# Performance work log

Measured on AMD Instinct MI355X. Metric: run time of the kernel, lower is better.

The kernel has to match this reference:

```python
import jax, jax.numpy as jnp
import numpy as np

D = 64          # embedding_dim
B = 1024        # batch (queries)
R = 128         # num_relations
N = 100000      # num_nodes
E = 6400000     # num_edges


def setup_inputs() -> dict:
    key = jax.random.key(0)
    ks = jax.random.split(key, 16)
    inp = {
        "relation_embeddings": jax.random.normal(ks[0], (B, R, D), dtype=jnp.float32),
        "query_rels": jax.random.randint(ks[1], (B,), 0, R),
        "query_entities": jax.random.randint(ks[2], (B,), 0, N),
        "edge_index": jax.random.randint(ks[3], (2, E), 0, N),
        "edge_type": jax.random.randint(ks[4], (E,), 0, R),
        "num_nodes": N,
        # feature_extractor: Linear(2D+4 -> D), ReLU, Linear(D -> D//2), ReLU
        "W1": jax.random.normal(ks[5], (2 * D + 4, D), dtype=jnp.float32) * 0.05,
        "b1": jnp.zeros((D,), dtype=jnp.float32),
        "W2": jax.random.normal(ks[6], (D, D // 2), dtype=jnp.float32) * 0.05,
        "b2": jnp.zeros((D // 2,), dtype=jnp.float32),
        # gate_network: Linear(D//2 -> D//4), ReLU, Linear(D//4 -> 1), Sigmoid
        "Wg1": jax.random.normal(ks[7], (D // 2, D // 4), dtype=jnp.float32) * 0.05,
        "bg1": jnp.zeros((D // 4,), dtype=jnp.float32),
        "Wg2": jax.random.normal(ks[8], (D // 4, 1), dtype=jnp.float32) * 0.05,
        "bg2": jnp.full((1,), 0.85, dtype=jnp.float32),
    }
    return inp


def reference(relation_embeddings, query_rels, query_entities, edge_index,
              edge_type, num_nodes, W1, b1, W2, b2, Wg1, bg1, Wg2, bg2):
    b, r, d = relation_embeddings.shape
    e = edge_type.shape[0]
    e_f = jnp.float32(e)
    src, dst = edge_index[0], edge_index[1]
    # count self-loop edges once (matches boolean OR mask in torch code)
    not_loop = (src != dst).astype(jnp.float32)

    # --- graph statistics (vectorized replacement of per-query masks) ---
    rel_counts = jnp.zeros((r,), jnp.float32).at[edge_type].add(1.0)          # [R]
    rel_freq_norm = jnp.minimum(rel_counts[query_rels] / e_f, 1.0)            # [B]

    deg = (jnp.zeros((num_nodes,), jnp.float32)
           .at[src].add(1.0).at[dst].add(not_loop))                           # [N]
    deg_q = deg[query_entities]                                               # [B]
    entity_degree_norm = jnp.minimum(deg_q / e_f, 1.0)

    density = jnp.minimum(e_f / jnp.float32(num_nodes * num_nodes), 1.0)
    stats = jnp.stack([rel_freq_norm, entity_degree_norm, rel_freq_norm,
                       jnp.full_like(rel_freq_norm, density)], axis=-1)       # [B,4]

    # --- query relation embedding ---
    rel_emb = relation_embeddings[jnp.arange(b), query_rels]                  # [B,D]

    # --- entity embedding = mean of relation embeddings over incident edges ---
    # per-node histogram of incident edge types (self loops counted once)
    hist = (jnp.zeros((num_nodes, r), jnp.float32)
            .at[src, edge_type].add(1.0)
            .at[dst, edge_type].add(not_loop))                                # [N,R]
    Mq = hist[query_entities]                                                 # [B,R]
    ent_sum = jnp.einsum('br,brd->bd', Mq, relation_embeddings)               # [B,D]
    entity_emb = ent_sum / jnp.maximum(deg_q, 1.0)[:, None]                   # zeros if deg==0

    # --- gated MLP ---
    feat = jnp.concatenate([rel_emb, entity_emb, stats], axis=-1)             # [B,2D+4]
    h = jax.nn.relu(feat @ W1 + b1)
    h = jax.nn.relu(h @ W2 + b2)
    g = jax.nn.relu(h @ Wg1 + bg1)
    gate = jax.nn.sigmoid(g @ Wg2 + bg2)[:, 0]                                # [B]
    return gate
```

## Files before the change

### kernel.cpp

```cpp
#include <hip/hip_runtime.h>
#include <math.h>


#define NNODES 100000
#define NWORDS ((NNODES + 31) / 32)
#define NWP    (((NWORDS + 3) / 4) * 4)
#define RR     128
#define DD     64
#define FF     (2 * DD + 4)
#define E4C    1600000
#define NTC    (512 * 1024)

__global__ void zero_kernel(int4* __restrict__ p, int n4)
{
    int i = blockIdx.x * blockDim.x + threadIdx.x;
    int stride = gridDim.x * blockDim.x;
    int4 z = make_int4(0, 0, 0, 0);
    for (int k = i; k < n4; k += stride) p[k] = z;
}

__global__ void __launch_bounds__(1024)
maskrank_kernel(const int* __restrict__ qents, int B,
                unsigned* __restrict__ gmask, int* __restrict__ gbase)
{
    __shared__ unsigned s_mask[NWP];
    __shared__ int s_sum[1024];
    int t = threadIdx.x;
    for (int k = t; k < NWP; k += 1024) s_mask[k] = 0u;
    __syncthreads();
    for (int b = t; b < B; b += 1024) {
        int e = qents[b];
        atomicOr(&s_mask[e >> 5], 1u << (e & 31));
    }
    __syncthreads();
    int w0 = t * 4;
    int pc[4]; int sum = 0;
    for (int k = 0; k < 4; ++k) {
        int w = w0 + k;
        unsigned mm = (w < NWP) ? s_mask[w] : 0u;
        pc[k] = __popc(mm);
        sum += pc[k];
    }
    s_sum[t] = sum;
    __syncthreads();
    for (int off = 1; off < 1024; off <<= 1) {
        int v = (t >= off) ? s_sum[t - off] : 0;
        __syncthreads();
        s_sum[t] += v;
        __syncthreads();
    }
    int base = s_sum[t] - sum;
    for (int k = 0; k < 4; ++k) {
        int w = w0 + k;
        if (w < NWP) gbase[w] = base;
        base += pc[k];
    }
    for (int k = t; k < NWP; k += 1024) gmask[k] = s_mask[k];
}

static __device__ __forceinline__ void edge1(
    int s, int d, int t, int* s_cnt,
    const unsigned* s_mask, const int* s_base,
    int* __restrict__ Mslot)
{
    atomicAdd(&s_cnt[t], 1);
    unsigned ws = s_mask[s >> 5];
    if ((ws >> (s & 31)) & 1u) {
        int slot = s_base[s >> 5] + __popc(ws & ((1u << (s & 31)) - 1u));
        atomicAdd(&Mslot[slot * RR + t], 1);
    }
    if (s != d) {
        unsigned wd = s_mask[d >> 5];
        if ((wd >> (d & 31)) & 1u) {
            int slot = s_base[d >> 5] + __popc(wd & ((1u << (d & 31)) - 1u));
            atomicAdd(&Mslot[slot * RR + t], 1);
        }
    }
}

static __device__ __forceinline__ void edge4(
    int4 s, int4 d, int4 t, int* s_cnt,
    const unsigned* s_mask, const int* s_base, int* __restrict__ Mslot)
{
    edge1(s.x, d.x, t.x, s_cnt, s_mask, s_base, Mslot);
    edge1(s.y, d.y, t.y, s_cnt, s_mask, s_base, Mslot);
    edge1(s.z, d.z, t.z, s_cnt, s_mask, s_base, Mslot);
    edge1(s.w, d.w, t.w, s_cnt, s_mask, s_base, Mslot);
}

__global__ void __launch_bounds__(1024, 8)
edge_kernel(const int* __restrict__ ei, const int* __restrict__ etype,
            int E, int E4,
            const unsigned* __restrict__ gmask, const int* __restrict__ gbase,
            int* __restrict__ Mslot, int* __restrict__ relcnt)
{
    __shared__ int s_cnt[RR];
    __shared__ __align__(16) unsigned s_mask[NWP];
    __shared__ __align__(16) int s_base[NWP];
    int t = threadIdx.x;
    if (t < RR) s_cnt[t] = 0;
    const uint4* gm4 = (const uint4*)gmask;
    const int4*  gb4 = (const int4*)gbase;
    for (int i = t; i < NWP / 4; i += 1024) {
        ((uint4*)s_mask)[i] = gm4[i];
        ((int4*)s_base)[i]  = gb4[i];
    }
    __syncthreads();

    int tid  = blockIdx.x * 1024 + t;
    int nthr = gridDim.x * 1024;

    const int4* src4 = (const int4*)ei;
    const int4* dst4 = (const int4*)(ei + E);
    const int4* et4  = (const int4*)etype;

    if (E4 == E4C && nthr == NTC) {
        int i0 = tid, i1 = tid + NTC, i2 = tid + 2 * NTC;
        int4 sa = src4[i0], da = dst4[i0], ta = et4[i0];
        int4 sb = src4[i1], db = dst4[i1], tb = et4[i1];
        int4 sc = src4[i2], dc = dst4[i2], tc = et4[i2];
        edge4(sa, da, ta, s_cnt, s_mask, s_base, Mslot);
        edge4(sb, db, tb, s_cnt, s_mask, s_base, Mslot);
        edge4(sc, dc, tc, s_cnt, s_mask, s_base, Mslot);
        int i3 = tid + 3 * NTC;
        if (i3 < E4C) {
            int4 sd = src4[i3], dd = dst4[i3], td = et4[i3];
            edge4(sd, dd, td, s_cnt, s_mask, s_base, Mslot);
        }
    } else {
        for (int i = tid; i < E4; i += nthr) {
            int4 s = src4[i], d = dst4[i], ty = et4[i];
            edge4(s, d, ty, s_cnt, s_mask, s_base, Mslot);
        }
        for (int e = (E4 << 2) + tid; e < E; e += nthr)
            edge1(ei[e], ei[E + e], etype[e], s_cnt, s_mask, s_base, Mslot);
    }

    __syncthreads();
    if (t < RR) {
        int c = s_cnt[t];
        if (c) atomicAdd(&relcnt[t], c);
    }
}

__global__ void query_kernel(
    const float* __restrict__ RE,
    const int* __restrict__ qrels, const int* __restrict__ qents,
    const int* __restrict__ relcnt, const int* __restrict__ Mslot,
    const unsigned* __restrict__ gmask, const int* __restrict__ gbase,
    const float* __restrict__ W1, const float* __restrict__ b1,
    const float* __restrict__ W2, const float* __restrict__ b2,
    const float* __restrict__ Wg1, const float* __restrict__ bg1,
    const float* __restrict__ Wg2, const float* __restrict__ bg2,
    float* __restrict__ out, float e_f, float density)
{
    __shared__ float s_m[RR];
    __shared__ float s_part[256];
    __shared__ float s_feat[FF];
    __shared__ float s_h1[DD];
    __shared__ float s_h2[DD / 2];
    __shared__ float s_g[DD / 4];
    __shared__ int s_slot;

    int b = blockIdx.x;
    int t = threadIdx.x;
    int d = t & (DD - 1);
    int w = t >> 6;

    if (t == 0) {
        int e = qents[b];
        unsigned mm = gmask[e >> 5];
        s_slot = gbase[e >> 5] + __popc(mm & ((1u << (e & 31)) - 1u));
    }
    __syncthreads();
    int slot = s_slot;

    if (t < RR) s_m[t] = (float)Mslot[slot * RR + t];
    __syncthreads();

    const float* REb = RE + (size_t)b * RR * DD;
    float acc = 0.f;
#pragma unroll 4
    for (int r = w; r < RR; r += 4) {
        float m = s_m[r];
        if (m != 0.f) acc = fmaf(m, REb[r * DD + d], acc);
    }
    s_part[w * DD + d] = acc;
    __syncthreads();

    if (t < DD) {
        float ds = s_m[t] + s_m[t + DD];
#pragma unroll
        for (int off = 32; off > 0; off >>= 1) ds += __shfl_xor(ds, off);

        float ent = s_part[t] + s_part[DD + t] + s_part[2 * DD + t] + s_part[3 * DD + t];

        int qr = qrels[b];
        s_feat[t]      = REb[qr * DD + t];
        s_feat[DD + t] = ent / fmaxf(ds, 1.f);
        if (t == 0) {
            float rf = fminf((float)relcnt[qr] / e_f, 1.f);
            s_feat[2 * DD + 0] = rf;
            s_feat[2 * DD + 1] = fminf(ds / e_f, 1.f);
            s_feat[2 * DD + 2] = rf;
            s_feat[2 * DD + 3] = density;
        }
    }
    __syncthreads();

    {
        int c = t >> 6, n = t & 63;
        int i0 = c * 33;
        float a = 0.f;
#pragma unroll
        for (int k = 0; k < 33; ++k) {
            int i = i0 + k;
            a = fmaf(s_feat[i], W1[i * DD + n], a);
        }
        s_part[t] = a;
    }
    __syncthreads();
    if (t < DD) {
        float a = b1[t] + s_part[t] + s_part[64 + t] + s_part[128 + t] + s_part[192 + t];
        s_h1[t] = fmaxf(a, 0.f);
    }
    __syncthreads();

    {
        int c = t >> 5, n = t & 31;
        float a = 0.f;
#pragma unroll
        for (int k = 0; k < 8; ++k) {
            int i = c * 8 + k;
            a = fmaf(s_h1[i], W2[i * 32 + n], a);
        }
        s_part[t] = a;
    }
    __syncthreads();
    if (t < 32) {
        float a = b2[t];
#pragma unroll
        for (int c = 0; c < 8; ++c) a += s_part[c * 32 + t];
        s_h2[t] = fmaxf(a, 0.f);
    }
    __syncthreads();

    if (t < 16) {
        float a = bg1[t];
#pragma unroll
        for (int i = 0; i < 32; ++i) a = fmaf(s_h2[i], Wg1[i * 16 + t], a);
        s_g[t] = fmaxf(a, 0.f);
    }
    __syncthreads();

    if (t == 0) {
        float a = bg2[0];
#pragma unroll
        for (int i = 0; i < 16; ++i) a = fmaf(s_g[i], Wg2[i], a);
        out[b] = 1.f / (1.f + expf(-a));
    }
}

extern "C" void kernel_launch(void* const* d_in, const int* in_sizes, int n_in,
                              void* d_out, int out_size, void* d_ws, size_t ws_size,
                              hipStream_t stream)
{
    const float* RE    = (const float*)d_in[0];
    const int*   qrels = (const int*)d_in[1];
    const int*   qents = (const int*)d_in[2];
    const int*   ei    = (const int*)d_in[3];
    const int*   etype = (const int*)d_in[4];
    const float* W1  = (const float*)d_in[6];
    const float* b1  = (const float*)d_in[7];
    const float* W2  = (const float*)d_in[8];
    const float* b2  = (const float*)d_in[9];
    const float* Wg1 = (const float*)d_in[10];
    const float* bg1 = (const float*)d_in[11];
    const float* Wg2 = (const float*)d_in[12];
    const float* bg2 = (const float*)d_in[13];
    float* out = (float*)d_out;

    int B = in_sizes[1];
    int E = in_sizes[4];

    int* ws_i   = (int*)d_ws;
    int* Mslot  = ws_i;
    int* relcnt = Mslot + (size_t)B * RR;
    unsigned* mask = (unsigned*)(relcnt + RR);
    int* word_base = (int*)(mask + NWP);

    float e_f = (float)E;
    float density = fminf((float)E / ((float)NNODES * (float)NNODES), 1.f);

    int n4 = (B * RR + RR) / 4;
    zero_kernel<<<256, 256, 0, stream>>>((int4*)d_ws, n4);

    maskrank_kernel<<<1, 1024, 0, stream>>>(qents, B, mask, word_base);

    int E4 = ((E & 3) == 0) ? (E >> 2) : 0;
    edge_kernel<<<512, 1024, 0, stream>>>(ei, etype, E, E4, mask, word_base,
                                          Mslot, relcnt);

    query_kernel<<<B, 256, 0, stream>>>(RE, qrels, qents, relcnt, Mslot,
                                        mask, word_base,
                                        W1, b1, W2, b2, Wg1, bg1, Wg2, bg2,
                                        out, e_f, density);
}
```

Measured before the change: 51.75 us.

## Fuse edge and query kernels via global flag barrier; merge zero and mask setup

Merges the zeroing kernel into the mask/rank setup kernel and replaces its block-wide scan with a wave-level shuffle scan. Fuses the edge scatter kernel and the per-query MLP kernel into one launch. Blocks signal completion through an atomic flag, and the first 256 blocks spin-wait on it before each handles 4 queries. This removes two launches and their inter-kernel gaps. It relies on all 512 blocks being co-resident to avoid deadlock, and reads the counters with atomics.

```diff
diff --git a/kernel.cpp b/kernel.cpp
--- a/kernel.cpp
+++ b/kernel.cpp
@@ -9,23 +9,25 @@
 #define DD     64
 #define FF     (2 * DD + 4)
 #define E4C    1600000
-#define NTC    (512 * 1024)
-
-__global__ void zero_kernel(int4* __restrict__ p, int n4)
-{
-    int i = blockIdx.x * blockDim.x + threadIdx.x;
-    int stride = gridDim.x * blockDim.x;
-    int4 z = make_int4(0, 0, 0, 0);
-    for (int k = i; k < n4; k += stride) p[k] = z;
-}
+#define EDGE_BLOCKS 512
+#define NTC    (EDGE_BLOCKS * 1024)
+#define QBLOCKS 256
 
 __global__ void __launch_bounds__(1024)
-maskrank_kernel(const int* __restrict__ qents, int B,
-                unsigned* __restrict__ gmask, int* __restrict__ gbase)
-{
+setup_kernel(const int* __restrict__ qents, int B,
+             unsigned* __restrict__ gmask, int* __restrict__ gbase,
+             int4* __restrict__ zp, int n4)
+{
+    int t = threadIdx.x;
+    if (blockIdx.x != 0) {
+        int i = (blockIdx.x - 1) * 1024 + t;
+        int stride = (gridDim.x - 1) * 1024;
+        int4 z = make_int4(0, 0, 0, 0);
+        for (int k = i; k < n4; k += stride) zp[k] = z;
+        return;
+    }
     __shared__ unsigned s_mask[NWP];
-    __shared__ int s_sum[1024];
-    int t = threadIdx.x;
+    __shared__ int s_wsum[16], s_wbase[16];
     for (int k = t; k < NWP; k += 1024) s_mask[k] = 0u;
     __syncthreads();
     for (int b = t; b < B; b += 1024) {
@@ -35,21 +37,30 @@
     __syncthreads();
     int w0 = t * 4;
     int pc[4]; int sum = 0;
+#pragma unroll
     for (int k = 0; k < 4; ++k) {
         int w = w0 + k;
         unsigned mm = (w < NWP) ? s_mask[w] : 0u;
         pc[k] = __popc(mm);
         sum += pc[k];
     }
-    s_sum[t] = sum;
-    __syncthreads();
-    for (int off = 1; off < 1024; off <<= 1) {
-        int v = (t >= off) ? s_sum[t - off] : 0;
-        __syncthreads();
-        s_sum[t] += v;
-        __syncthreads();
-    }
-    int base = s_sum[t] - sum;
+    int lane = t & 63, wid = t >> 6;
+    int incl = sum;
+#pragma unroll
+    for (int off = 1; off < 64; off <<= 1) {
+        int v = __shfl_up(incl, off);
+        if (lane >= off) incl += v;
+    }
+    if (lane == 63) s_wsum[wid] = incl;
+    __syncthreads();
+    if (t == 0) {
+        int run = 0;
+#pragma unroll
+        for (int k = 0; k < 16; ++k) { s_wbase[k] = run; run += s_wsum[k]; }
+    }
+    __syncthreads();
+    int base = s_wbase[wid] + incl - sum;
+#pragma unroll
     for (int k = 0; k < 4; ++k) {
         int w = w0 + k;
         if (w < NWP) gbase[w] = base;
@@ -59,44 +70,60 @@
 }
 
 static __device__ __forceinline__ void edge1(
-    int s, int d, int t, int* s_cnt,
+    int s, int d, int ty, int* s_cnt,
     const unsigned* s_mask, const int* s_base,
     int* __restrict__ Mslot)
 {
-    atomicAdd(&s_cnt[t], 1);
+    atomicAdd(&s_cnt[ty], 1);
     unsigned ws = s_mask[s >> 5];
     if ((ws >> (s & 31)) & 1u) {
         int slot = s_base[s >> 5] + __popc(ws & ((1u << (s & 31)) - 1u));
-        atomicAdd(&Mslot[slot * RR + t], 1);
+        atomicAdd(&Mslot[slot * RR + ty], 1);
     }
     if (s != d) {
         unsigned wd = s_mask[d >> 5];
         if ((wd >> (d & 31)) & 1u) {
             int slot = s_base[d >> 5] + __popc(wd & ((1u << (d & 31)) - 1u));
-            atomicAdd(&Mslot[slot * RR + t], 1);
+            atomicAdd(&Mslot[slot * RR + ty], 1);
         }
     }
 }
 
 static __device__ __forceinline__ void edge4(
-    int4 s, int4 d, int4 t, int* s_cnt,
+    int4 s, int4 d, int4 ty, int* s_cnt,
     const unsigned* s_mask, const int* s_base, int* __restrict__ Mslot)
 {
-    edge1(s.x, d.x, t.x, s_cnt, s_mask, s_base, Mslot);
-    edge1(s.y, d.y, t.y, s_cnt, s_mask, s_base, Mslot);
-    edge1(s.z, d.z, t.z, s_cnt, s_mask, s_base, Mslot);
-    edge1(s.w, d.w, t.w, s_cnt, s_mask, s_base, Mslot);
+    edge1(s.x, d.x, ty.x, s_cnt, s_mask, s_base, Mslot);
+    edge1(s.y, d.y, ty.y, s_cnt, s_mask, s_base, Mslot);
+    edge1(s.z, d.z, ty.z, s_cnt, s_mask, s_base, Mslot);
+    edge1(s.w, d.w, ty.w, s_cnt, s_mask, s_base, Mslot);
 }
 
 __global__ void __launch_bounds__(1024, 8)
-edge_kernel(const int* __restrict__ ei, const int* __restrict__ etype,
-            int E, int E4,
-            const unsigned* __restrict__ gmask, const int* __restrict__ gbase,
-            int* __restrict__ Mslot, int* __restrict__ relcnt)
+fused_kernel(const int* __restrict__ ei, const int* __restrict__ etype,
+             int E, int E4,
+             const unsigned* __restrict__ gmask, const int* __restrict__ gbase,
+             int* __restrict__ Mslot, int* __restrict__ relcnt,
+             int* __restrict__ flag,
+             const float* __restrict__ RE,
+             const int* __restrict__ qrels, const int* __restrict__ qents,
+             const float* __restrict__ W1, const float* __restrict__ b1,
+             const float* __restrict__ W2, const float* __restrict__ b2,
+             const float* __restrict__ Wg1, const float* __restrict__ bg1,
+             const float* __restrict__ Wg2, const float* __restrict__ bg2,
+             float* __restrict__ out, int B, float e_f, float density)
 {
     __shared__ int s_cnt[RR];
     __shared__ __align__(16) unsigned s_mask[NWP];
     __shared__ __align__(16) int s_base[NWP];
+    __shared__ float qs_m[4][RR];
+    __shared__ float qs_part[4][256];
+    __shared__ float qs_feat[4][FF];
+    __shared__ float qs_h1[4][DD];
+    __shared__ float qs_h2[4][DD / 2];
+    __shared__ float qs_g[4][DD / 4];
+    __shared__ int qs_slot[4];
+
     int t = threadIdx.x;
     if (t < RR) s_cnt[t] = 0;
     const uint4* gm4 = (const uint4*)gmask;
@@ -141,123 +168,116 @@
         int c = s_cnt[t];
         if (c) atomicAdd(&relcnt[t], c);
     }
-}
-
-__global__ void query_kernel(
-    const float* __restrict__ RE,
-    const int* __restrict__ qrels, const int* __restrict__ qents,
-    const int* __restrict__ relcnt, const int* __restrict__ Mslot,
-    const unsigned* __restrict__ gmask, const int* __restrict__ gbase,
-    const float* __restrict__ W1, const float* __restrict__ b1,
-    const float* __restrict__ W2, const float* __restrict__ b2,
-    const float* __restrict__ Wg1, const float* __restrict__ bg1,
-    const float* __restrict__ Wg2, const float* __restrict__ bg2,
-    float* __restrict__ out, float e_f, float density)
-{
-    __shared__ float s_m[RR];
-    __shared__ float s_part[256];
-    __shared__ float s_feat[FF];
-    __shared__ float s_h1[DD];
-    __shared__ float s_h2[DD / 2];
-    __shared__ float s_g[DD / 4];
-    __shared__ int s_slot;
-
-    int b = blockIdx.x;
-    int t = threadIdx.x;
-    int d = t & (DD - 1);
-    int w = t >> 6;
+    __syncthreads();
+    if (t == 0) { __threadfence(); atomicAdd(flag, 1); }
+    if (blockIdx.x >= QBLOCKS) return;
 
     if (t == 0) {
-        int e = qents[b];
-        unsigned mm = gmask[e >> 5];
-        s_slot = gbase[e >> 5] + __popc(mm & ((1u << (e & 31)) - 1u));
-    }
-    __syncthreads();
-    int slot = s_slot;
-
-    if (t < RR) s_m[t] = (float)Mslot[slot * RR + t];
-    __syncthreads();
-
-    const float* REb = RE + (size_t)b * RR * DD;
+        while (atomicAdd(flag, 0) < (int)gridDim.x)
+            __builtin_amdgcn_s_sleep(8);
+        __threadfence();
+    }
+    __syncthreads();
+
+    int sub = t >> 8, tl = t & 255;
+    int q = blockIdx.x * 4 + sub;
+    if (q >= B) q = B - 1;
+    int d = tl & (DD - 1);
+    int w = tl >> 6;
+
+    if (tl == 0) {
+        int e = qents[q];
+        unsigned mm = s_mask[e >> 5];
+        qs_slot[sub] = s_base[e >> 5] + __popc(mm & ((1u << (e & 31)) - 1u));
+    }
+    __syncthreads();
+    int slot = qs_slot[sub];
+
+    if (tl < RR) qs_m[sub][tl] = (float)atomicAdd(&Mslot[slot * RR + tl], 0);
+    __syncthreads();
+
+    const float* REq = RE + (size_t)q * RR * DD;
     float acc = 0.f;
 #pragma unroll 4
     for (int r = w; r < RR; r += 4) {
-        float m = s_m[r];
-        if (m != 0.f) acc = fmaf(m, REb[r * DD + d], acc);
-    }
-    s_part[w * DD + d] = acc;
-    __syncthreads();
-
-    if (t < DD) {
-        float ds = s_m[t] + s_m[t + DD];
+        float m = qs_m[sub][r];
+        if (m != 0.f) acc = fmaf(m, REq[r * DD + d], acc);
+    }
+    qs_part[sub][w * DD + d] = acc;
+    __syncthreads();
+
+    if (tl < DD) {
+        float ds = qs_m[sub][tl] + qs_m[sub][tl + DD];
 #pragma unroll
         for (int off = 32; off > 0; off >>= 1) ds += __shfl_xor(ds, off);
 
-        float ent = s_part[t] + s_part[DD + t] + s_part[2 * DD + t] + s_part[3 * DD + t];
-
-        int qr = qrels[b];
-        s_feat[t]      = REb[qr * DD + t];
-        s_feat[DD + t] = ent / fmaxf(ds, 1.f);
-        if (t == 0) {
-            float rf = fminf((float)relcnt[qr] / e_f, 1.f);
-            s_feat[2 * DD + 0] = rf;
-            s_feat[2 * DD + 1] = fminf(ds / e_f, 1.f);
-            s_feat[2 * DD + 2] = rf;
-            s_feat[2 * DD + 3] = density;
+        float ent = qs_part[sub][tl] + qs_part[sub][DD + tl]
+                  + qs_part[sub][2 * DD + tl] + qs_part[sub][3 * DD + tl];
+
+        int qr = qrels[q];
+        qs_feat[sub][tl]      = REq[qr * DD + tl];
+        qs_feat[sub][DD + tl] = ent / fmaxf(ds, 1.f);
+        if (tl == 0) {
+            float rf = fminf((float)atomicAdd(&relcnt[qr], 0) / e_f, 1.f);
+            qs_feat[sub][2 * DD + 0] = rf;
+            qs_feat[sub][2 * DD + 1] = fminf(ds / e_f, 1.f);
+            qs_feat[sub][2 * DD + 2] = rf;
+            qs_feat[sub][2 * DD + 3] = density;
         }
     }
     __syncthreads();
 
     {
-        int c = t >> 6, n = t & 63;
+        int c = tl >> 6, n = tl & 63;
         int i0 = c * 33;
         float a = 0.f;
 #pragma unroll
         for (int k = 0; k < 33; ++k) {
             int i = i0 + k;
-            a = fmaf(s_feat[i], W1[i * DD + n], a);
-        }
-        s_part[t] = a;
-    }
-    __syncthreads();
-    if (t < DD) {
-        float a = b1[t] + s_part[t] + s_part[64 + t] + s_part[128 + t] + s_part[192 + t];
-        s_h1[t] = fmaxf(a, 0.f);
+            a = fmaf(qs_feat[sub][i], W1[i * DD + n], a);
+        }
+        qs_part[sub][tl] = a;
+    }
+    __syncthreads();
+    if (tl < DD) {
+        float a = b1[tl] + qs_part[sub][tl] + qs_part[sub][64 + tl]
+                + qs_part[sub][128 + tl] + qs_part[sub][192 + tl];
+        qs_h1[sub][tl] = fmaxf(a, 0.f);
     }
     __syncthreads();
 
     {
-        int c = t >> 5, n = t & 31;
+        int c = tl >> 5, n = tl & 31;
         float a = 0.f;
 #pragma unroll
         for (int k = 0; k < 8; ++k) {
             int i = c * 8 + k;
-            a = fmaf(s_h1[i], W2[i * 32 + n], a);
-        }
-        s_part[t] = a;
-    }
-    __syncthreads();
-    if (t < 32) {
-        float a = b2[t];
-#pragma unroll
-        for (int c = 0; c < 8; ++c) a += s_part[c * 32 + t];
-        s_h2[t] = fmaxf(a, 0.f);
-    }
-    __syncthreads();
-
-    if (t < 16) {
-        float a = bg1[t];
-#pragma unroll
-        for (int i = 0; i < 32; ++i) a = fmaf(s_h2[i], Wg1[i * 16 + t], a);
-        s_g[t] = fmaxf(a, 0.f);
-    }
-    __syncthreads();
-
-    if (t == 0) {
+            a = fmaf(qs_h1[sub][i], W2[i * 32 + n], a);
+        }
+        qs_part[sub][tl] = a;
+    }
+    __syncthreads();
+    if (tl < 32) {
+        float a = b2[tl];
+#pragma unroll
+        for (int c = 0; c < 8; ++c) a += qs_part[sub][c * 32 + tl];
+        qs_h2[sub][tl] = fmaxf(a, 0.f);
+    }
+    __syncthreads();
+
+    if (tl < 16) {
+        float a = bg1[tl];
+#pragma unroll
+        for (int i = 0; i < 32; ++i) a = fmaf(qs_h2[sub][i], Wg1[i * 16 + tl], a);
+        qs_g[sub][tl] = fmaxf(a, 0.f);
+    }
+    __syncthreads();
+
+    if (tl == 0) {
         float a = bg2[0];
 #pragma unroll
-        for (int i = 0; i < 16; ++i) a = fmaf(s_g[i], Wg2[i], a);
-        out[b] = 1.f / (1.f + expf(-a));
+        for (int i = 0; i < 16; ++i) a = fmaf(qs_g[sub][i], Wg2[i], a);
+        out[q] = 1.f / (1.f + expf(-a));
     }
 }
 
@@ -286,23 +306,21 @@
     int* ws_i   = (int*)d_ws;
     int* Mslot  = ws_i;
     int* relcnt = Mslot + (size_t)B * RR;
-    unsigned* mask = (unsigned*)(relcnt + RR);
+    int* flag   = relcnt + RR;
+    unsigned* mask = (unsigned*)(flag + 4);
     int* word_base = (int*)(mask + NWP);
 
     float e_f = (float)E;
     float density = fminf((float)E / ((float)NNODES * (float)NNODES), 1.f);
 
-    int n4 = (B * RR + RR) / 4;
-    zero_kernel<<<256, 256, 0, stream>>>((int4*)d_ws, n4);
-
-    maskrank_kernel<<<1, 1024, 0, stream>>>(qents, B, mask, word_base);
+    int n4 = (B * RR + RR + 4) / 4;
+
+    setup_kernel<<<64, 1024, 0, stream>>>(qents, B, mask, word_base,
+                                          (int4*)d_ws, n4);
 
     int E4 = ((E & 3) == 0) ? (E >> 2) : 0;
-    edge_kernel<<<512, 1024, 0, stream>>>(ei, etype, E, E4, mask, word_base,
-                                          Mslot, relcnt);
-
-    query_kernel<<<B, 256, 0, stream>>>(RE, qrels, qents, relcnt, Mslot,
-                                        mask, word_base,
-                                        W1, b1, W2, b2, Wg1, bg1, Wg2, bg2,
-                                        out, e_f, density);
-}
+    fused_kernel<<<EDGE_BLOCKS, 1024, 0, stream>>>(
+        ei, etype, E, E4, mask, word_base, Mslot, relcnt, flag,
+        RE, qrels, qents, W1, b1, W2, b2, Wg1, bg1, Wg2, bg2,
+        out, B, e_f, density);
+}
```

Measured after the change: 87.06 us. 1.68x slower.

## Merge zero and mask-rank kernels, use wave-shuffle scan, buffer hits in LDS

Applied to the files above, without the earlier changes.

Folds the workspace-zeroing kernel into the mask/rank kernel as extra blocks, which removes one launch. The block-wide prefix scan now uses wave shuffles plus a 16-entry cross-wave pass instead of a barrier-heavy Hillis-Steele loop over shared memory. In the edge kernel, hits on query nodes are appended to a per-block LDS buffer and flushed to global Mslot atomics after the barrier, so the global atomic traffic is no longer interleaved with the edge loop. The cost is a contended shared counter atomic per hit and more LDS per block. That extra LDS may reduce occupancy.

```diff
diff --git a/kernel.cpp b/kernel.cpp
--- a/kernel.cpp
+++ b/kernel.cpp
@@ -9,23 +9,25 @@
 #define DD     64
 #define FF     (2 * DD + 4)
 #define E4C    1600000
-#define NTC    (512 * 1024)
-
-__global__ void zero_kernel(int4* __restrict__ p, int n4)
-{
-    int i = blockIdx.x * blockDim.x + threadIdx.x;
-    int stride = gridDim.x * blockDim.x;
-    int4 z = make_int4(0, 0, 0, 0);
-    for (int k = i; k < n4; k += stride) p[k] = z;
-}
+#define EDGE_BLOCKS 512
+#define NTC    (EDGE_BLOCKS * 1024)
+#define HITCAP 2048
 
 __global__ void __launch_bounds__(1024)
-maskrank_kernel(const int* __restrict__ qents, int B,
-                unsigned* __restrict__ gmask, int* __restrict__ gbase)
-{
+setup_kernel(const int* __restrict__ qents, int B,
+             unsigned* __restrict__ gmask, int* __restrict__ gbase,
+             int4* __restrict__ zp, int n4)
+{
+    int t = threadIdx.x;
+    if (blockIdx.x != 0) {
+        int i = (blockIdx.x - 1) * 1024 + t;
+        int stride = (gridDim.x - 1) * 1024;
+        int4 z = make_int4(0, 0, 0, 0);
+        for (int k = i; k < n4; k += stride) zp[k] = z;
+        return;
+    }
     __shared__ unsigned s_mask[NWP];
-    __shared__ int s_sum[1024];
-    int t = threadIdx.x;
+    __shared__ int s_wsum[16], s_wbase[16];
     for (int k = t; k < NWP; k += 1024) s_mask[k] = 0u;
     __syncthreads();
     for (int b = t; b < B; b += 1024) {
@@ -35,21 +37,30 @@
     __syncthreads();
     int w0 = t * 4;
     int pc[4]; int sum = 0;
+#pragma unroll
     for (int k = 0; k < 4; ++k) {
         int w = w0 + k;
         unsigned mm = (w < NWP) ? s_mask[w] : 0u;
         pc[k] = __popc(mm);
         sum += pc[k];
     }
-    s_sum[t] = sum;
-    __syncthreads();
-    for (int off = 1; off < 1024; off <<= 1) {
-        int v = (t >= off) ? s_sum[t - off] : 0;
-        __syncthreads();
-        s_sum[t] += v;
-        __syncthreads();
-    }
-    int base = s_sum[t] - sum;
+    int lane = t & 63, wid = t >> 6;
+    int incl = sum;
+#pragma unroll
+    for (int off = 1; off < 64; off <<= 1) {
+        int v = __shfl_up(incl, off);
+        if (lane >= off) incl += v;
+    }
+    if (lane == 63) s_wsum[wid] = incl;
+    __syncthreads();
+    if (t == 0) {
+        int run = 0;
+#pragma unroll
+        for (int k = 0; k < 16; ++k) { s_wbase[k] = run; run += s_wsum[k]; }
+    }
+    __syncthreads();
+    int base = s_wbase[wid] + incl - sum;
+#pragma unroll
     for (int k = 0; k < 4; ++k) {
         int w = w0 + k;
         if (w < NWP) gbase[w] = base;
@@ -59,33 +70,38 @@
 }
 
 static __device__ __forceinline__ void edge1(
-    int s, int d, int t, int* s_cnt,
+    int s, int d, int ty, int* s_cnt,
     const unsigned* s_mask, const int* s_base,
-    int* __restrict__ Mslot)
-{
-    atomicAdd(&s_cnt[t], 1);
+    unsigned* s_hit, int* s_hn, int* __restrict__ Mslot)
+{
+    atomicAdd(&s_cnt[ty], 1);
     unsigned ws = s_mask[s >> 5];
     if ((ws >> (s & 31)) & 1u) {
         int slot = s_base[s >> 5] + __popc(ws & ((1u << (s & 31)) - 1u));
-        atomicAdd(&Mslot[slot * RR + t], 1);
+        int idx = atomicAdd(s_hn, 1);
+        if (idx < HITCAP) s_hit[idx] = (unsigned)(slot * RR + ty);
+        else atomicAdd(&Mslot[slot * RR + ty], 1);
     }
     if (s != d) {
         unsigned wd = s_mask[d >> 5];
         if ((wd >> (d & 31)) & 1u) {
             int slot = s_base[d >> 5] + __popc(wd & ((1u << (d & 31)) - 1u));
-            atomicAdd(&Mslot[slot * RR + t], 1);
+            int idx = atomicAdd(s_hn, 1);
+            if (idx < HITCAP) s_hit[idx] = (unsigned)(slot * RR + ty);
+            else atomicAdd(&Mslot[slot * RR + ty], 1);
         }
     }
 }
 
 static __device__ __forceinline__ void edge4(
-    int4 s, int4 d, int4 t, int* s_cnt,
-    const unsigned* s_mask, const int* s_base, int* __restrict__ Mslot)
-{
-    edge1(s.x, d.x, t.x, s_cnt, s_mask, s_base, Mslot);
-    edge1(s.y, d.y, t.y, s_cnt, s_mask, s_base, Mslot);
-    edge1(s.z, d.z, t.z, s_cnt, s_mask, s_base, Mslot);
-    edge1(s.w, d.w, t.w, s_cnt, s_mask, s_base, Mslot);
+    int4 s, int4 d, int4 ty, int* s_cnt,
+    const unsigned* s_mask, const int* s_base,
+    unsigned* s_hit, int* s_hn, int* __restrict__ Mslot)
+{
+    edge1(s.x, d.x, ty.x, s_cnt, s_mask, s_base, s_hit, s_hn, Mslot);
+    edge1(s.y, d.y, ty.y, s_cnt, s_mask, s_base, s_hit, s_hn, Mslot);
+    edge1(s.z, d.z, ty.z, s_cnt, s_mask, s_base, s_hit, s_hn, Mslot);
+    edge1(s.w, d.w, ty.w, s_cnt, s_mask, s_base, s_hit, s_hn, Mslot);
 }
 
 __global__ void __launch_bounds__(1024, 8)
@@ -97,8 +113,11 @@
     __shared__ int s_cnt[RR];
     __shared__ __align__(16) unsigned s_mask[NWP];
     __shared__ __align__(16) int s_base[NWP];
+    __shared__ unsigned s_hit[HITCAP];
+    __shared__ int s_hn;
     int t = threadIdx.x;
     if (t < RR) s_cnt[t] = 0;
+    if (t == 0) s_hn = 0;
     const uint4* gm4 = (const uint4*)gmask;
     const int4*  gb4 = (const int4*)gbase;
     for (int i = t; i < NWP / 4; i += 1024) {
@@ -119,24 +138,28 @@
         int4 sa = src4[i0], da = dst4[i0], ta = et4[i0];
         int4 sb = src4[i1], db = dst4[i1], tb = et4[i1];
         int4 sc = src4[i2], dc = dst4[i2], tc = et4[i2];
-        edge4(sa, da, ta, s_cnt, s_mask, s_base, Mslot);
-        edge4(sb, db, tb, s_cnt, s_mask, s_base, Mslot);
-        edge4(sc, dc, tc, s_cnt, s_mask, s_base, Mslot);
+        edge4(sa, da, ta, s_cnt, s_mask, s_base, s_hit, &s_hn, Mslot);
+        edge4(sb, db, tb, s_cnt, s_mask, s_base, s_hit, &s_hn, Mslot);
+        edge4(sc, dc, tc, s_cnt, s_mask, s_base, s_hit, &s_hn, Mslot);
         int i3 = tid + 3 * NTC;
         if (i3 < E4C) {
             int4 sd = src4[i3], dd = dst4[i3], td = et4[i3];
-            edge4(sd, dd, td, s_cnt, s_mask, s_base, Mslot);
+            edge4(sd, dd, td, s_cnt, s_mask, s_base, s_hit, &s_hn, Mslot);
         }
     } else {
         for (int i = tid; i < E4; i += nthr) {
             int4 s = src4[i], d = dst4[i], ty = et4[i];
-            edge4(s, d, ty, s_cnt, s_mask, s_base, Mslot);
+            edge4(s, d, ty, s_cnt, s_mask, s_base, s_hit, &s_hn, Mslot);
         }
         for (int e = (E4 << 2) + tid; e < E; e += nthr)
-            edge1(ei[e], ei[E + e], etype[e], s_cnt, s_mask, s_base, Mslot);
-    }
-
-    __syncthreads();
+            edge1(ei[e], ei[E + e], etype[e], s_cnt, s_mask, s_base,
+                  s_hit, &s_hn, Mslot);
+    }
+
+    __syncthreads();
+    int hn = s_hn; if (hn > HITCAP) hn = HITCAP;
+    for (int i = t; i < hn; i += 1024)
+        atomicAdd(&Mslot[s_hit[i]], 1);
     if (t < RR) {
         int c = s_cnt[t];
         if (c) atomicAdd(&relcnt[t], c);
@@ -293,13 +316,14 @@
     float density = fminf((float)E / ((float)NNODES * (float)NNODES), 1.f);
 
     int n4 = (B * RR + RR) / 4;
-    zero_kernel<<<256, 256, 0, stream>>>((int4*)d_ws, n4);
-
-    maskrank_kernel<<<1, 1024, 0, stream>>>(qents, B, mask, word_base);
+
+    setup_kernel<<<64, 1024, 0, stream>>>(qents, B, mask, word_base,
+                                          (int4*)d_ws, n4);
 
     int E4 = ((E & 3) == 0) ? (E >> 2) : 0;
-    edge_kernel<<<512, 1024, 0, stream>>>(ei, etype, E, E4, mask, word_base,
-                                          Mslot, relcnt);
+    edge_kernel<<<EDGE_BLOCKS, 1024, 0, stream>>>(ei, etype, E, E4,
+                                                  mask, word_base,
+                                                  Mslot, relcnt);
 
     query_kernel<<<B, 256, 0, stream>>>(RE, qrels, qents, relcnt, Mslot,
                                         mask, word_base,
```

Result: faster. 48.03 us (-7.2%).
